# Optimization experiments

Measured on AMD Instinct MI355X. Metric: run time of the kernel, lower is better.

Reference implementation:

```python
import jax, jax.numpy as jnp
import numpy as np

EMBED = 1024
HEADS = 16
HEAD_DIM = EMBED // HEADS


def setup_inputs() -> dict:
    key = jax.random.key(0)
    ks = jax.random.split(key, 11)
    B, S = 4, 2048
    scale = 0.02
    inp = {
        "value": jax.random.normal(ks[0], (B, S, EMBED), jnp.float32),
        "key": jax.random.normal(ks[1], (B, S, EMBED), jnp.float32),
        "query": jax.random.normal(ks[2], (B, S, EMBED), jnp.float32),
        "Wv": jax.random.normal(ks[3], (EMBED, EMBED), jnp.float32) * scale,
        "bv": jax.random.normal(ks[4], (EMBED,), jnp.float32) * scale,
        "Wk": jax.random.normal(ks[5], (EMBED, EMBED), jnp.float32) * scale,
        "bk": jax.random.normal(ks[6], (EMBED,), jnp.float32) * scale,
        "Wq": jax.random.normal(ks[7], (EMBED, EMBED), jnp.float32) * scale,
        "bq": jax.random.normal(ks[8], (EMBED,), jnp.float32) * scale,
        "Wo": jax.random.normal(ks[9], (EMBED, EMBED), jnp.float32) * scale,
        "bo": jax.random.normal(ks[10], (EMBED,), jnp.float32) * scale,
    }
    return inp


def reference(value, key, query, Wv, bv, Wk, bk, Wq, bq, Wo, bo):
    B, Sq, E = query.shape
    # linear projections (torch Linear: x @ W.T + b; here W stored as [in, out])
    v = (value @ Wv + bv).reshape(B, -1, HEADS, HEAD_DIM)   # [B,Skv,H,D]
    k = (key @ Wk + bk).reshape(B, -1, HEADS, HEAD_DIM)
    q = (query @ Wq + bq).reshape(B, Sq, HEADS, HEAD_DIM)
    # scaled dot-product attention, full score matrix [B,H,Sq,Skv]
    energy = jnp.einsum("bqhd,bkhd->bhqk", q, k) / jnp.sqrt(jnp.float32(HEAD_DIM))
    attn = jax.nn.softmax(energy, axis=-1)
    out = jnp.einsum("bhqk,bkhd->bqhd", attn, v).reshape(B, Sq, E)
    return out @ Wo + bo
```

## Files before the change

kernel.cpp:

```cpp
#include <hip/hip_runtime.h>
#include <hip/hip_bf16.h>
#include <stdint.h>

typedef unsigned short u16;
typedef __bf16 bf16_t;
typedef bf16_t bf16x8 __attribute__((ext_vector_type(8)));
typedef float f32x4 __attribute__((ext_vector_type(4)));

__device__ __forceinline__ u16 f2b(float f) {
    union { float f; uint32_t i; } v; v.f = f;
    uint32_t r = v.i + 0x7FFFu + ((v.i >> 16) & 1u);
    return (u16)(r >> 16);
}
__device__ __forceinline__ uint32_t pk2(float a, float b) {
    __hip_bfloat162 h = __float22bfloat162_rn(float2{a, b});
    return *(const uint32_t*)&h;
}
__device__ __forceinline__ uint4 pack8(float4 lo, float4 hi) {
    uint4 r;
    r.x = pk2(lo.x, lo.y); r.y = pk2(lo.z, lo.w);
    r.z = pk2(hi.x, hi.y); r.w = pk2(hi.z, hi.w);
    return r;
}
__device__ __forceinline__ void async16(const u16* g, u16* l) {
    __builtin_amdgcn_global_load_lds(
        (const __attribute__((address_space(1))) uint32_t*)g,
        (__attribute__((address_space(3))) uint32_t*)l,
        16, 0, 0);
}

template<bool XF32>
__device__ __forceinline__ void gemm128(const void* __restrict__ Xv,
                                        const u16* __restrict__ WT,
                                        const float* __restrict__ bias,
                                        u16* __restrict__ dstb,
                                        float* __restrict__ dstf, int mode)
{
    __shared__ __align__(16) u16 As[128 * 64];
    __shared__ __align__(16) u16 Bs[128 * 64];
    const int t    = threadIdx.x;
    const int lane = t & 63;
    const int quad = lane >> 4;
    const int l15  = lane & 15;
    const int m0 = blockIdx.y * 128;
    const int n0 = blockIdx.x * 128;
    const int wave = t >> 6;
    const int wm = (wave >> 1) * 64;
    const int wn = (wave & 1) * 64;

    f32x4 acc[4][4];
#pragma unroll
    for (int i = 0; i < 4; i++)
#pragma unroll
        for (int j = 0; j < 4; j++)
#pragma unroll
            for (int r = 0; r < 4; r++) acc[i][j][r] = 0.0f;

    int rr[4], lb[4];
#pragma unroll
    for (int c = 0; c < 4; c++) {
        const int ci = c * 256 + t;
        rr[c] = ci >> 3;
        lb[c] = (ci & 7) ^ (rr[c] & 7);
    }

    for (int kt = 0; kt < 1024; kt += 64) {
        __syncthreads();
#pragma unroll
        for (int c = 0; c < 4; c++)
            async16(WT + (n0 + rr[c]) * 1024 + kt + lb[c] * 8, &Bs[(c * 256 + t) * 8]);
        if (XF32) {
#pragma unroll
            for (int c = 0; c < 4; c++) {
                const float* g = (const float*)Xv + (m0 + rr[c]) * 1024 + kt + lb[c] * 8;
                const float4 lo = *(const float4*)g;
                const float4 hi = *(const float4*)(g + 4);
                *(uint4*)&As[(c * 256 + t) * 8] = pack8(lo, hi);
            }
        } else {
#pragma unroll
            for (int c = 0; c < 4; c++)
                async16((const u16*)Xv + (m0 + rr[c]) * 1024 + kt + lb[c] * 8,
                        &As[(c * 256 + t) * 8]);
        }
        __syncthreads();

#pragma unroll
        for (int kk = 0; kk < 64; kk += 32) {
            bf16x8 af[4], bfv[4];
#pragma unroll
            for (int i = 0; i < 4; i++) {
                const int ra = wm + i * 16 + l15;
                const int rb2 = wn + i * 16 + l15;
                af[i]  = *(const bf16x8*)&As[ra * 64 + (((kk >> 3) + quad) ^ (l15 & 7)) * 8];
                bfv[i] = *(const bf16x8*)&Bs[rb2 * 64 + (((kk >> 3) + quad) ^ (l15 & 7)) * 8];
            }
#pragma unroll
            for (int i = 0; i < 4; i++)
#pragma unroll
                for (int j = 0; j < 4; j++)
                    acc[i][j] = __builtin_amdgcn_mfma_f32_16x16x32_bf16(af[i], bfv[j], acc[i][j], 0, 0, 0);
        }
    }

#pragma unroll
    for (int i = 0; i < 4; i++) {
        const int rb = m0 + wm + i * 16 + quad * 4;
#pragma unroll
        for (int j = 0; j < 4; j++) {
            const int col = n0 + wn + j * 16 + l15;
            const float bias_v = bias[col];
            if (mode == 2) {
                const int b = rb >> 11, s = rb & 2047;
                const int h = col >> 6, d = col & 63;
                uint2 pk;
                pk.x = pk2(acc[i][j][0] + bias_v, acc[i][j][1] + bias_v);
                pk.y = pk2(acc[i][j][2] + bias_v, acc[i][j][3] + bias_v);
                *(uint2*)&dstb[((b * 16 + h) * 64 + d) * 2048 + s] = pk;
            } else {
#pragma unroll
                for (int r = 0; r < 4; r++) {
                    const float v = acc[i][j][r] + bias_v;
                    const int gm = rb + r;
                    if (mode == 0) {
                        const int b = gm >> 11, s = gm & 2047;
                        const int h = col >> 6, d = col & 63;
                        dstb[((b * 16 + h) * 2048 + s) * 64 + d] = f2b(v);
                    } else {
                        dstf[gm * 1024 + col] = v;
                    }
                }
            }
        }
    }
}

__global__ __launch_bounds__(256)
void convert_x(const float* __restrict__ q_in, const float* __restrict__ k_in,
               const float* __restrict__ v_in, u16* __restrict__ Xb)
{
    const int z = blockIdx.y;
    const float* src = (z == 0) ? q_in : (z == 1) ? k_in : v_in;
    u16* dst = Xb + z * (8 * 1024 * 1024);
    const int i = (blockIdx.x * 256 + threadIdx.x) * 8;
    const float4 lo = *(const float4*)(src + i);
    const float4 hi = *(const float4*)(src + i + 4);
    *(uint4*)(dst + i) = pack8(lo, hi);
}

__global__ __launch_bounds__(256)
void qkv_kernel_f32(const float* __restrict__ q_in, const float* __restrict__ k_in,
                    const float* __restrict__ v_in, const u16* __restrict__ WT,
                    const float* __restrict__ bq, const float* __restrict__ bk,
                    const float* __restrict__ bv,
                    u16* __restrict__ Qo, u16* __restrict__ Ko, u16* __restrict__ VTo)
{
    const int z = blockIdx.z;
    const float* X   = (z == 0) ? q_in : (z == 1) ? k_in : v_in;
    const u16* wt    = WT + ((z == 0) ? 2 : (z == 1) ? 1 : 0) * (1024 * 1024);
    const float* bias= (z == 0) ? bq : (z == 1) ? bk : bv;
    u16* dst         = (z == 0) ? Qo : (z == 1) ? Ko : VTo;
    gemm128<true>(X, wt, bias, dst, nullptr, (z == 2) ? 2 : 0);
}

__global__ __launch_bounds__(256)
void qkv_kernel_b16(const u16* __restrict__ Xb, const u16* __restrict__ WT,
                    const float* __restrict__ bq, const float* __restrict__ bk,
                    const float* __restrict__ bv,
                    u16* __restrict__ Qo, u16* __restrict__ Ko, u16* __restrict__ VTo)
{
    const int z = blockIdx.z;
    const u16* X     = Xb + z * (8 * 1024 * 1024);
    const u16* wt    = WT + ((z == 0) ? 2 : (z == 1) ? 1 : 0) * (1024 * 1024);
    const float* bias= (z == 0) ? bq : (z == 1) ? bk : bv;
    u16* dst         = (z == 0) ? Qo : (z == 1) ? Ko : VTo;
    gemm128<false>(X, wt, bias, dst, nullptr, (z == 2) ? 2 : 0);
}

__global__ __launch_bounds__(256)
void oproj_kernel(const u16* __restrict__ AO, const u16* __restrict__ WT,
                  const float* __restrict__ bo, float* __restrict__ out)
{
    gemm128<false>(AO, WT + 3 * 1024 * 1024, bo, nullptr, out, 1);
}

__global__ void transpose_w(const float* __restrict__ Wv, const float* __restrict__ Wk,
                            const float* __restrict__ Wq, const float* __restrict__ Wo,
                            u16* __restrict__ WT)
{
    __shared__ u16 tile[64][65];
    const int z = blockIdx.z;
    const float* W = (z == 0) ? Wv : (z == 1) ? Wk : (z == 2) ? Wq : Wo;
    u16* dst = WT + z * 1024 * 1024;
    const int r0 = blockIdx.y * 64, c0 = blockIdx.x * 64;
    const int col = threadIdx.x & 63, rb = threadIdx.x >> 6;
#pragma unroll
    for (int r = rb; r < 64; r += 4) tile[r][col] = f2b(W[(r0 + r) * 1024 + c0 + col]);
    __syncthreads();
#pragma unroll
    for (int r = rb; r < 64; r += 4) dst[(c0 + r) * 1024 + r0 + col] = tile[col][r];
}

__global__ __launch_bounds__(256, 3)
void attn_kernel(const u16* __restrict__ Q, const u16* __restrict__ K,
                 const u16* __restrict__ VT, u16* __restrict__ AO)
{
    __shared__ __align__(16) u16 Ks[128 * 64];
    __shared__ __align__(16) u16 Ps[64 * 128];
    __shared__ __align__(16) u16 Vts[80 * 128];

    const int t    = threadIdx.x;
    const int lane = t & 63;
    const int wave = t >> 6;
    const int quad = lane >> 4;
    const int l15  = lane & 15;
    const int bh = blockIdx.y;
    const int qt = blockIdx.x;

    const u16* Qg = Q + (bh * 2048 + qt * 64) * 64;
    const u16* Kg = K + bh * 2048 * 64;
    const u16* Vg = VT + bh * 64 * 2048;

    const u16* kgp[4];
    const u16* vgp[4];
    u16* kld[4];
    u16* vld[4];
#pragma unroll
    for (int c = 0; c < 4; c++) {
        const int ci = c * 256 + t;
        const int krr = ci >> 3, klb = (ci & 7)  ^ (krr & 7);
        const int vrr = ci >> 4, vlb = (ci & 15) ^ (vrr & 15);
        kgp[c] = Kg + krr * 64 + klb * 8;
        vgp[c] = Vg + vrr * 2048 + vlb * 8;
        kld[c] = &Ks[ci * 8];
        vld[c] = &Vts[ci * 8];
    }

#pragma unroll
    for (int c = 0; c < 4; c++) {
        async16(kgp[c], kld[c]);
        kgp[c] += 128 * 64;
    }

    {
        const int idx = t * 8;
        const int row = 64 + (idx >> 7);
        const u16 one = 0x3F80;
        u16 vals[8];
#pragma unroll
        for (int i = 0; i < 8; i++) vals[i] = (row == 64) ? one : (u16)0;
        *(uint4*)&Vts[64 * 128 + idx] = *(uint4*)vals;
    }

    bf16x8 bqr[2];
    {
        const u16* qrow = Qg + (wave * 16 + l15) * 64 + quad * 8;
#pragma unroll
        for (int c = 0; c < 2; c++) {
            uint4 dv = *(const uint4*)(qrow + c * 32);
            u16 tmp[8];
            *(uint4*)tmp = dv;
            float f[8];
#pragma unroll
            for (int i = 0; i < 8; i++) {
                union { float f; uint32_t u; } x; x.u = ((uint32_t)tmp[i]) << 16;
                f[i] = x.f * 0.18033688f;
            }
            uint4 pk;
            pk.x = pk2(f[0], f[1]); pk.y = pk2(f[2], f[3]);
            pk.z = pk2(f[4], f[5]); pk.w = pk2(f[6], f[7]);
            bqr[c] = *(bf16x8*)&pk;
        }
    }

    f32x4 o[5];
#pragma unroll
    for (int dj = 0; dj < 5; dj++)
#pragma unroll
        for (int r = 0; r < 4; r++) o[dj][r] = 0.0f;
    float m_st = 0.0f;

    int ak_off[2][8];
#pragma unroll
    for (int ki = 0; ki < 2; ki++)
#pragma unroll
        for (int n = 0; n < 8; n++)
            ak_off[ki][n] = (n * 16 + l15) * 64 + (((ki * 4) + quad) ^ (l15 & 7)) * 8;
    int av_off[4][5], bp_off[4], pw_off[8];
#pragma unroll
    for (int ks = 0; ks < 4; ks++) {
        bp_off[ks] = (wave * 16 + l15) * 128 + ((ks * 4 + quad) ^ l15) * 8;
#pragma unroll
        for (int dj = 0; dj < 5; dj++)
            av_off[ks][dj] = (dj * 16 + l15) * 128 + ((ks * 4 + quad) ^ l15) * 8;
    }
#pragma unroll
    for (int n = 0; n < 8; n++)
        pw_off[n] = (wave * 16 + l15) * 128 + ((2 * n + (quad >> 1)) ^ l15) * 8
                    + (quad & 1) * 4;

    for (int kv = 0; kv < 16; kv++) {
        __syncthreads();
#pragma unroll
        for (int c = 0; c < 4; c++) {
            async16(vgp[c], vld[c]);
            vgp[c] += 128;
        }

        f32x4 s[8];
#pragma unroll
        for (int n = 0; n < 8; n++)
#pragma unroll
            for (int r = 0; r < 4; r++) s[n][r] = -m_st;
#pragma unroll
        for (int ki = 0; ki < 2; ki++) {
            const bf16x8 bq = bqr[ki];
#pragma unroll
            for (int n = 0; n < 8; n++) {
                const bf16x8 ak = *(const bf16x8*)&Ks[ak_off[ki][n]];
                s[n] = __builtin_amdgcn_mfma_f32_16x16x32_bf16(ak, bq, s[n], 0, 0, 0);
            }
        }

        __syncthreads();
        if (kv < 15) {
#pragma unroll
            for (int c = 0; c < 4; c++) {
                async16(kgp[c], kld[c]);
                kgp[c] += 128 * 64;
            }
        }

        float mxn[8];
#pragma unroll
        for (int n = 0; n < 8; n++)
            mxn[n] = fmaxf(fmaxf(s[n][0], s[n][1]), fmaxf(s[n][2], s[n][3]));
        float mx = fmaxf(fmaxf(fmaxf(mxn[0], mxn[1]), fmaxf(mxn[2], mxn[3])),
                         fmaxf(fmaxf(mxn[4], mxn[5]), fmaxf(mxn[6], mxn[7])));
        mx = fmaxf(mx, __shfl_xor(mx, 16));
        mx = fmaxf(mx, __shfl_xor(mx, 32));
        if (__any(mx > 8.0f)) {
            const float dm = fmaxf(mx, 0.0f);
            const float alpha = exp2f(-dm);
#pragma unroll
            for (int n = 0; n < 8; n++)
#pragma unroll
                for (int r = 0; r < 4; r++) s[n][r] -= dm;
            m_st += dm;
#pragma unroll
            for (int dj = 0; dj < 5; dj++)
#pragma unroll
                for (int r = 0; r < 4; r++) o[dj][r] *= alpha;
        }

#pragma unroll
        for (int n = 0; n < 8; n++) {
            uint2 pk;
            pk.x = pk2(exp2f(s[n][0]), exp2f(s[n][1]));
            pk.y = pk2(exp2f(s[n][2]), exp2f(s[n][3]));
            *(uint2*)&Ps[pw_off[n]] = pk;
        }
        asm volatile("s_waitcnt lgkmcnt(0)" ::: "memory");

#pragma unroll
        for (int ks = 0; ks < 4; ks++) {
            const bf16x8 bp = *(const bf16x8*)&Ps[bp_off[ks]];
#pragma unroll
            for (int dj = 0; dj < 5; dj++) {
                const bf16x8 av = *(const bf16x8*)&Vts[av_off[ks][dj]];
                o[dj] = __builtin_amdgcn_mfma_f32_16x16x32_bf16(av, bp, o[dj], 0, 0, 0);
            }
        }
    }

    const float lsum = __shfl(o[4][0], l15);
    const int b = bh >> 4, h = bh & 15;
    const int sq = qt * 64 + wave * 16 + l15;
    const float inv = 1.0f / lsum;
#pragma unroll
    for (int dj = 0; dj < 4; dj++) {
        uint2 pk;
        pk.x = pk2(o[dj][0] * inv, o[dj][1] * inv);
        pk.y = pk2(o[dj][2] * inv, o[dj][3] * inv);
        *(uint2*)&AO[(b * 2048 + sq) * 1024 + h * 64 + dj * 16 + quad * 4] = pk;
    }
}

extern "C" void kernel_launch(void* const* d_in, const int* in_sizes, int n_in,
                              void* d_out, int out_size, void* d_ws, size_t ws_size,
                              hipStream_t stream)
{
    (void)in_sizes; (void)n_in; (void)out_size;
    const float* value = (const float*)d_in[0];
    const float* key_  = (const float*)d_in[1];
    const float* query = (const float*)d_in[2];
    const float* Wv = (const float*)d_in[3];
    const float* bv = (const float*)d_in[4];
    const float* Wk = (const float*)d_in[5];
    const float* bk = (const float*)d_in[6];
    const float* Wq = (const float*)d_in[7];
    const float* bq = (const float*)d_in[8];
    const float* Wo = (const float*)d_in[9];
    const float* bo = (const float*)d_in[10];

    u16* ws = (u16*)d_ws;
    u16* WT = ws;
    u16* Q  = ws + 4 * 1024 * 1024;
    u16* K  = Q + 8 * 1024 * 1024;
    u16* VT = K + 8 * 1024 * 1024;
    u16* AO = VT + 8 * 1024 * 1024;
    u16* Xb = AO + 8 * 1024 * 1024;
    const size_t need = (size_t)(4 + 8 + 8 + 8 + 8 + 24) * 1024 * 1024 * sizeof(u16);

    transpose_w<<<dim3(16, 16, 4), dim3(256), 0, stream>>>(Wv, Wk, Wq, Wo, WT);
    if (ws_size >= need) {
        convert_x<<<dim3(4096, 3), dim3(256), 0, stream>>>(query, key_, value, Xb);
        qkv_kernel_b16<<<dim3(8, 64, 3), dim3(256), 0, stream>>>(Xb, WT, bq, bk, bv,
                                                                 Q, K, VT);
    } else {
        qkv_kernel_f32<<<dim3(8, 64, 3), dim3(256), 0, stream>>>(query, key_, value,
                                                                 WT, bq, bk, bv,
                                                                 Q, K, VT);
    }
    attn_kernel<<<dim3(32, 64), dim3(256), 0, stream>>>(Q, K, VT, AO);
    oproj_kernel<<<dim3(8, 64, 1), dim3(256), 0, stream>>>(AO, WT, bo, (float*)d_out);
}
```

Before: 398.2 us.

## Swizzle GEMM tile order and trim per-iteration softmax overhead in attention

```diff
diff --git a/kernel.cpp b/kernel.cpp
--- a/kernel.cpp
+++ b/kernel.cpp
@@ -34,7 +34,8 @@
                                         const u16* __restrict__ WT,
                                         const float* __restrict__ bias,
                                         u16* __restrict__ dstb,
-                                        float* __restrict__ dstf, int mode)
+                                        float* __restrict__ dstf, int mode,
+                                        int m0, int n0)
 {
     __shared__ __align__(16) u16 As[128 * 64];
     __shared__ __align__(16) u16 Bs[128 * 64];
@@ -42,8 +43,6 @@
     const int lane = t & 63;
     const int quad = lane >> 4;
     const int l15  = lane & 15;
-    const int m0 = blockIdx.y * 128;
-    const int n0 = blockIdx.x * 128;
     const int wave = t >> 6;
     const int wm = (wave >> 1) * 64;
     const int wn = (wave & 1) * 64;
@@ -160,7 +159,8 @@
     const u16* wt    = WT + ((z == 0) ? 2 : (z == 1) ? 1 : 0) * (1024 * 1024);
     const float* bias= (z == 0) ? bq : (z == 1) ? bk : bv;
     u16* dst         = (z == 0) ? Qo : (z == 1) ? Ko : VTo;
-    gemm128<true>(X, wt, bias, dst, nullptr, (z == 2) ? 2 : 0);
+    gemm128<true>(X, wt, bias, dst, nullptr, (z == 2) ? 2 : 0,
+                  blockIdx.y * 128, blockIdx.x * 128);
 }
 
 __global__ __launch_bounds__(256)
@@ -174,14 +174,20 @@
     const u16* wt    = WT + ((z == 0) ? 2 : (z == 1) ? 1 : 0) * (1024 * 1024);
     const float* bias= (z == 0) ? bq : (z == 1) ? bk : bv;
     u16* dst         = (z == 0) ? Qo : (z == 1) ? Ko : VTo;
-    gemm128<false>(X, wt, bias, dst, nullptr, (z == 2) ? 2 : 0);
+    const int s = blockIdx.y * 8 + blockIdx.x;
+    const int o = (s & 7) * 64 + (s >> 3);
+    gemm128<false>(X, wt, bias, dst, nullptr, (z == 2) ? 2 : 0,
+                   (o >> 3) * 128, (o & 7) * 128);
 }
 
 __global__ __launch_bounds__(256)
 void oproj_kernel(const u16* __restrict__ AO, const u16* __restrict__ WT,
                   const float* __restrict__ bo, float* __restrict__ out)
 {
-    gemm128<false>(AO, WT + 3 * 1024 * 1024, bo, nullptr, out, 1);
+    const int s = blockIdx.y * 8 + blockIdx.x;
+    const int o = (s & 7) * 64 + (s >> 3);
+    gemm128<false>(AO, WT + 3 * 1024 * 1024, bo, nullptr, out, 1,
+                   (o >> 3) * 128, (o & 7) * 128);
 }
 
 __global__ void transpose_w(const float* __restrict__ Wv, const float* __restrict__ Wk,
@@ -279,6 +285,9 @@
 #pragma unroll
         for (int r = 0; r < 4; r++) o[dj][r] = 0.0f;
     float m_st = 0.0f;
+    f32x4 cinit;
+#pragma unroll
+    for (int r = 0; r < 4; r++) cinit[r] = 0.0f;
 
     int ak_off[2][8];
 #pragma unroll
@@ -310,17 +319,12 @@
         f32x4 s[8];
 #pragma unroll
         for (int n = 0; n < 8; n++)
-#pragma unroll
-            for (int r = 0; r < 4; r++) s[n][r] = -m_st;
-#pragma unroll
-        for (int ki = 0; ki < 2; ki++) {
-            const bf16x8 bq = bqr[ki];
-#pragma unroll
-            for (int n = 0; n < 8; n++) {
-                const bf16x8 ak = *(const bf16x8*)&Ks[ak_off[ki][n]];
-                s[n] = __builtin_amdgcn_mfma_f32_16x16x32_bf16(ak, bq, s[n], 0, 0, 0);
-            }
-        }
+            s[n] = __builtin_amdgcn_mfma_f32_16x16x32_bf16(
+                *(const bf16x8*)&Ks[ak_off[0][n]], bqr[0], cinit, 0, 0, 0);
+#pragma unroll
+        for (int n = 0; n < 8; n++)
+            s[n] = __builtin_amdgcn_mfma_f32_16x16x32_bf16(
+                *(const bf16x8*)&Ks[ak_off[1][n]], bqr[1], s[n], 0, 0, 0);
 
         __syncthreads();
         if (kv < 15) {
@@ -337,9 +341,9 @@
             mxn[n] = fmaxf(fmaxf(s[n][0], s[n][1]), fmaxf(s[n][2], s[n][3]));
         float mx = fmaxf(fmaxf(fmaxf(mxn[0], mxn[1]), fmaxf(mxn[2], mxn[3])),
                          fmaxf(fmaxf(mxn[4], mxn[5]), fmaxf(mxn[6], mxn[7])));
-        mx = fmaxf(mx, __shfl_xor(mx, 16));
-        mx = fmaxf(mx, __shfl_xor(mx, 32));
         if (__any(mx > 8.0f)) {
+            mx = fmaxf(mx, __shfl_xor(mx, 16));
+            mx = fmaxf(mx, __shfl_xor(mx, 32));
             const float dm = fmaxf(mx, 0.0f);
             const float alpha = exp2f(-dm);
 #pragma unroll
@@ -347,6 +351,8 @@
 #pragma unroll
                 for (int r = 0; r < 4; r++) s[n][r] -= dm;
             m_st += dm;
+#pragma unroll
+            for (int r = 0; r < 4; r++) cinit[r] = -m_st;
 #pragma unroll
             for (int dj = 0; dj < 5; dj++)
 #pragma unroll
```

After: 380.2 us. -4.5%, faster.
